# Kernel optimization log

Measured on AMD Instinct MI355X. Metric: run time of the kernel, lower is better.

Reference implementation:

```python
import jax, jax.numpy as jnp
import numpy as np

B, H, S, D = 4, 16, 2048, 128


def setup_inputs() -> dict:
    key = jax.random.key(0)
    kq, kk, kv = jax.random.split(key, 3)
    query = jax.random.normal(kq, (B, H, S, D), dtype=jnp.float32)
    key_t = jax.random.normal(kk, (B, H, S, D), dtype=jnp.float32)
    value = jax.random.normal(kv, (B, H, S, D), dtype=jnp.float32)
    # causal mask, broadcast over batch and heads: True = keep
    mask = jnp.tril(jnp.ones((S, S), dtype=bool))[None, None].repeat(B, 0).repeat(H, 1)
    return {"query": query, "key": key_t, "value": value, "mask": mask}


def reference(query, key, value, mask):
    scale = 1.0 / np.sqrt(D).astype(np.float32)
    # [b,h,sq,sk] scores
    scores = jnp.einsum("bhqd,bhkd->bhqk", query, key) * scale
    scores = jnp.where(mask, scores, -jnp.inf)
    probs = jax.nn.softmax(scores, axis=-1)
    return jnp.einsum("bhqk,bhkd->bhqd", probs, value)
```

## Files before the change

### kernel.cpp

```cpp
#include <hip/hip_runtime.h>


#define SLEN 2048
#define DDIM 128
#define NBH  64
#define QB   256
#define KB   64

typedef __bf16 bf16x8 __attribute__((ext_vector_type(8)));
typedef float  f32x16 __attribute__((ext_vector_type(16)));
typedef float  f32x4  __attribute__((ext_vector_type(4)));
typedef unsigned uint32x4 __attribute__((ext_vector_type(4)));
typedef unsigned short ushort_t;
typedef ushort_t ushort8 __attribute__((ext_vector_type(8)));

__device__ inline ushort_t f2bf(float f) {
  union { float f; unsigned u; } v; v.f = f;
  unsigned u = v.u;
  u += 0x7FFFu + ((u >> 16) & 1u);
  return (ushort_t)(u >> 16);
}

__device__ inline unsigned cvtpk_bf16(float lo, float hi) {
  unsigned r;
  asm("v_cvt_pk_bf16_f32 %0, %1, %2" : "=v"(r) : "v"(lo), "v"(hi));
  return r;
}

__device__ inline float exp2_fast(float x) {
  float r;
  asm("v_exp_f32 %0, %1" : "=v"(r) : "v"(x));
  return r;
}

__global__ __launch_bounds__(256) void prepass_kernel(
    const float* __restrict__ K, const float* __restrict__ V,
    ushort_t* __restrict__ Kb, ushort_t* __restrict__ Vt) {
  __shared__ float t[64][33];
  if (blockIdx.x < 2048) {
    const int n4 = (int)((size_t)NBH * SLEN * DDIM / 4);
    const int stride = 2048 * 256;
    for (int i = blockIdx.x * 256 + threadIdx.x; i < n4; i += stride) {
      float4 x = reinterpret_cast<const float4*>(K)[i];
      unsigned lo = (unsigned)f2bf(x.x) | ((unsigned)f2bf(x.y) << 16);
      unsigned hi = (unsigned)f2bf(x.z) | ((unsigned)f2bf(x.w) << 16);
      reinterpret_cast<uint2*>(Kb)[i] = make_uint2(lo, hi);
    }
  } else {
    const int vb = (int)blockIdx.x - 2048;
    const int bh = vb >> 7;
    const int d0 = ((vb >> 5) & 3) * 32;
    const int s0 = (vb & 31) * 64;
    const int tx = threadIdx.x & 31;
    const int ty = threadIdx.x >> 5;
    const float* src = V + ((size_t)bh * SLEN + s0) * DDIM + d0;
#pragma unroll
    for (int j = 0; j < 8; ++j) {
      int sl = ty + j * 8;
      t[sl][tx] = src[(size_t)sl * DDIM + tx];
    }
    __syncthreads();
    ushort_t* dst = Vt + ((size_t)bh * DDIM + d0) * SLEN + s0;
#pragma unroll
    for (int j = 0; j < 4; ++j) {
      int dl = ty + j * 8;
      unsigned lo = f2bf(t[tx * 2][dl]);
      unsigned hi = f2bf(t[tx * 2 + 1][dl]);
      *reinterpret_cast<unsigned*>(&dst[(size_t)dl * SLEN + tx * 2]) =
          lo | (hi << 16);
    }
  }
}

#define QKT(S, TT) do {                                                      \
    const int _b = (TT) % 3;                                                 \
    _Pragma("unroll")                                                        \
    for (int mt = 0; mt < 2; ++mt) {                                         \
      f32x16 a;                                                              \
      _Pragma("unroll")                                                      \
      for (int r = 0; r < 16; ++r) a[r] = 0.f;                               \
      int row = mt * 32 + l31;                                               \
      int sw = row & 7;                                                      \
      _Pragma("unroll")                                                      \
      for (int ds = 0; ds < 8; ++ds) {                                       \
        int c = ds * 2 + hi;                                                 \
        bf16x8 kf = *reinterpret_cast<const bf16x8*>(                        \
            &K_sh[_b][row * DDIM + ((c ^ sw) << 3)]);                        \
        a = __builtin_amdgcn_mfma_f32_32x32x16_bf16(kf, qf[ds], a, 0, 0, 0); \
      }                                                                      \
      S[mt] = a;                                                             \
    }                                                                        \
  } while (0)

#define FINISH(S, U) do {                                                    \
    const int _u = (U);                                                      \
    const int _vb = _u % 3;                                                  \
    if (_u * 64 + 63 > q0w) {                                                \
      _Pragma("unroll")                                                      \
      for (int mt = 0; mt < 2; ++mt) {                                       \
        int kbase = _u * 64 + mt * 32 + 4 * hi;                              \
        _Pragma("unroll")                                                    \
        for (int r = 0; r < 16; ++r) {                                       \
          int krow = (r & 3) + 8 * (r >> 2);                                 \
          if (kbase + krow > qg) S[mt][r] = -3.0e38f;                        \
        }                                                                    \
      }                                                                      \
    }                                                                        \
    float p0 = S[0][0], p1 = S[0][1], p2 = S[0][2], p3 = S[0][3];            \
    _Pragma("unroll")                                                        \
    for (int r = 4; r < 16; r += 4) {                                        \
      p0 = fmaxf(p0, S[0][r]);     p1 = fmaxf(p1, S[0][r + 1]);              \
      p2 = fmaxf(p2, S[0][r + 2]); p3 = fmaxf(p3, S[0][r + 3]);              \
    }                                                                        \
    _Pragma("unroll")                                                        \
    for (int r = 0; r < 16; r += 4) {                                        \
      p0 = fmaxf(p0, S[1][r]);     p1 = fmaxf(p1, S[1][r + 1]);              \
      p2 = fmaxf(p2, S[1][r + 2]); p3 = fmaxf(p3, S[1][r + 3]);              \
    }                                                                        \
    float tm = fmaxf(fmaxf(p0, p1), fmaxf(p2, p3));                          \
    tm = fmaxf(tm, __shfl_xor(tm, 32));                                      \
    if (!__all(tm - m_run <= THR)) {                                         \
      float mnew  = fmaxf(m_run, tm);                                        \
      float alpha = exp2_fast(m_run - mnew);                                 \
      m_run = mnew; l_run *= alpha;                                          \
      _Pragma("unroll")                                                      \
      for (int dt = 0; dt < 4; ++dt)                                         \
        _Pragma("unroll")                                                    \
        for (int r = 0; r < 16; ++r) Oacc[dt][r] *= alpha;                   \
    }                                                                        \
    float s0 = 0.f, s1 = 0.f, s2 = 0.f, s3 = 0.f;                            \
    _Pragma("unroll")                                                        \
    for (int mt = 0; mt < 2; ++mt)                                           \
      _Pragma("unroll")                                                      \
      for (int r = 0; r < 16; r += 4) {                                      \
        float e0 = exp2_fast(S[mt][r + 0] - m_run);                          \
        float e1 = exp2_fast(S[mt][r + 1] - m_run);                          \
        float e2 = exp2_fast(S[mt][r + 2] - m_run);                          \
        float e3 = exp2_fast(S[mt][r + 3] - m_run);                          \
        S[mt][r + 0] = e0; S[mt][r + 1] = e1;                                \
        S[mt][r + 2] = e2; S[mt][r + 3] = e3;                                \
        s0 += e0; s1 += e1; s2 += e2; s3 += e3;                              \
      }                                                                      \
    float rs = (s0 + s1) + (s2 + s3);                                        \
    rs += __shfl_xor(rs, 32);                                                \
    l_run += rs;                                                             \
    uint32x4 pw[4];                                                          \
    _Pragma("unroll")                                                        \
    for (int ks = 0; ks < 4; ++ks) {                                         \
      const int mt = ks >> 1;                                                \
      const int hb = 8 * (ks & 1);                                           \
      unsigned X  = cvtpk_bf16(S[mt][hb + 0], S[mt][hb + 1]);                \
      unsigned X2 = cvtpk_bf16(S[mt][hb + 2], S[mt][hb + 3]);                \
      unsigned Y  = cvtpk_bf16(S[mt][hb + 4], S[mt][hb + 5]);                \
      unsigned Y2 = cvtpk_bf16(S[mt][hb + 6], S[mt][hb + 7]);                \
      asm("v_permlane32_swap_b32 %0, %1" : "+v"(X),  "+v"(Y));               \
      asm("v_permlane32_swap_b32 %0, %1" : "+v"(X2), "+v"(Y2));              \
      uint32x4 f; f.x = X; f.y = X2; f.z = Y; f.w = Y2;                      \
      pw[ks] = f;                                                            \
    }                                                                        \
    _Pragma("unroll")                                                        \
    for (int dt = 0; dt < 4; ++dt) {                                         \
      int row = dt * 32 + l31;                                               \
      int sw = row & 7;                                                      \
      __builtin_amdgcn_s_setprio(1);                                         \
      _Pragma("unroll")                                                      \
      for (int ks = 0; ks < 4; ++ks) {                                       \
        int c = ks * 2 + hi;                                                 \
        bf16x8 vf = *reinterpret_cast<const bf16x8*>(                        \
            &V_sh[_vb][row * 64 + ((c ^ sw) << 3)]);                         \
        Oacc[dt] = __builtin_amdgcn_mfma_f32_32x32x16_bf16(                  \
            vf, __builtin_bit_cast(bf16x8, pw[ks]), Oacc[dt], 0, 0, 0);      \
      }                                                                      \
      __builtin_amdgcn_s_setprio(0);                                         \
    }                                                                        \
  } while (0)

__global__ __launch_bounds__(512, 1) void fattn6_kernel(
    const float* __restrict__ Q, const ushort_t* __restrict__ Kb,
    const ushort_t* __restrict__ Vt, float* __restrict__ Out) {
  __shared__ ushort_t K_sh[3][KB * DDIM];
  __shared__ ushort_t V_sh[3][DDIM * KB];

  const int tid  = threadIdx.x;
  const int lane = tid & 63;
  const int wv   = tid >> 6;
  const int l31  = lane & 31;
  const int hi   = lane >> 5;
  const int qblk = (blockIdx.y >= 32) ? blockIdx.x : (7 - (int)blockIdx.x);
  const int bh   = blockIdx.y;

  const float qscale = 0.12751744f;
  const float THR = 11.0f;

  const float*    Qp = Q  + (size_t)bh * SLEN * DDIM;
  const ushort_t* Kp = Kb + (size_t)bh * SLEN * DDIM;
  const ushort_t* Vp = Vt + (size_t)bh * DDIM * SLEN;
  float*          Op = Out + (size_t)bh * SLEN * DDIM;

  const int q0w = qblk * QB + wv * 32;
  const int qg  = q0w + l31;

  bf16x8 qf[8];
  {
    const float* qr = Qp + (size_t)qg * DDIM;
#pragma unroll
    for (int ds = 0; ds < 8; ++ds) {
      int d0 = ds * 16 + hi * 8;
      float4 x = *reinterpret_cast<const float4*>(qr + d0);
      float4 y = *reinterpret_cast<const float4*>(qr + d0 + 4);
      ushort8 uu;
      uu[0] = f2bf(x.x * qscale); uu[1] = f2bf(x.y * qscale);
      uu[2] = f2bf(x.z * qscale); uu[3] = f2bf(x.w * qscale);
      uu[4] = f2bf(y.x * qscale); uu[5] = f2bf(y.y * qscale);
      uu[6] = f2bf(y.z * qscale); uu[7] = f2bf(y.w * qscale);
      qf[ds] = __builtin_bit_cast(bf16x8, uu);
    }
  }

  f32x16 Oacc[4];
#pragma unroll
  for (int dt = 0; dt < 4; ++dt)
#pragma unroll
    for (int r = 0; r < 16; ++r) Oacc[dt][r] = 0.f;
  float m_run = -3.0e38f, l_run = 0.f;

  const int last_kb = qblk * 4 + 3;
  const int lkw     = 4 * qblk + (wv >> 1);

  auto stage = [&](int buf, int kb) {
    const ushort_t* ksrc = Kp + (size_t)kb * KB * DDIM;
#pragma unroll
    for (int j = 0; j < 2; ++j) {
      int chunk = wv * 128 + j * 64 + lane;
      int row = chunk >> 4, c = chunk & 15;
      const ushort_t* g = ksrc + row * DDIM + ((c ^ (row & 7)) << 3);
      ushort_t* l = &K_sh[buf][(wv * 128 + j * 64) * 8];
      __builtin_amdgcn_global_load_lds(
          (const __attribute__((address_space(1))) unsigned*)g,
          (__attribute__((address_space(3))) unsigned*)l, 16, 0, 0);
    }
    const ushort_t* vsrc = Vp + (size_t)kb * KB;
#pragma unroll
    for (int j = 0; j < 2; ++j) {
      int chunk = wv * 128 + j * 64 + lane;
      int row = chunk >> 3, c = chunk & 7;
      const ushort_t* g = vsrc + (size_t)row * SLEN + ((c ^ (row & 7)) << 3);
      ushort_t* l = &V_sh[buf][(wv * 128 + j * 64) * 8];
      __builtin_amdgcn_global_load_lds(
          (const __attribute__((address_space(1))) unsigned*)g,
          (__attribute__((address_space(3))) unsigned*)l, 16, 0, 0);
    }
  };

  f32x16 sacA[2], sacB[2];

  stage(0, 0);

  __syncthreads();
  stage(1, 1);
  QKT(sacA, 0);

  __syncthreads();
  if (1 < last_kb) stage(2, 2);
  if (1 <= lkw)           { QKT(sacB, 1); FINISH(sacA, 0); }
  else if (lkw == 0)      { FINISH(sacA, 0); }

  for (int t = 2; t <= last_kb; t += 2) {
    __syncthreads();
    if (t < last_kb) stage((t + 1) % 3, t + 1);
    if (t <= lkw)            { QKT(sacA, t); FINISH(sacB, t - 1); }
    else if (t == lkw + 1)   { FINISH(sacB, t - 1); }

    __syncthreads();
    if (t + 1 < last_kb) stage((t + 2) % 3, t + 2);
    if (t + 1 <= lkw)          { QKT(sacB, t + 1); FINISH(sacA, t); }
    else if (t + 1 == lkw + 1) { FINISH(sacA, t); }
  }

  if (lkw == last_kb) { FINISH(sacB, last_kb); }

  {
    float invl = 1.0f / l_run;
    float* orow = Op + (size_t)qg * DDIM;
#pragma unroll
    for (int dt = 0; dt < 4; ++dt)
#pragma unroll
      for (int rq = 0; rq < 4; ++rq) {
        float4 o;
        o.x = Oacc[dt][rq * 4 + 0] * invl;
        o.y = Oacc[dt][rq * 4 + 1] * invl;
        o.z = Oacc[dt][rq * 4 + 2] * invl;
        o.w = Oacc[dt][rq * 4 + 3] * invl;
        int d = dt * 32 + 8 * rq + 4 * hi;
        *reinterpret_cast<float4*>(orow + d) = o;
      }
  }
}

__global__ __launch_bounds__(256) void fattn_kernel(
    const float* __restrict__ Q, const float* __restrict__ K,
    const float* __restrict__ V, float* __restrict__ Out) {
  __shared__ ushort_t Kf_sh[64 * 128];
  __shared__ ushort_t Vf_sh[128 * 64];
  __shared__ ushort_t P_sh[4][16 * 64];

  const int tid  = threadIdx.x;
  const int lane = tid & 63;
  const int wv   = tid >> 6;
  const int l16  = lane & 15;
  const int lhi  = lane >> 4;
  const int qblk = blockIdx.x;
  const int bh   = blockIdx.y;
  const float scale = 0.08838834764831845f;

  const size_t base = (size_t)bh * SLEN * DDIM;
  const float* Qp = Q + base;
  const float* Kp = K + base;
  const float* Vp = V + base;
  float*       Op = Out + base;

  bf16x8 qf[4];
  {
    const int qrow = qblk * 64 + wv * 16 + l16;
    const float* qr = Qp + (size_t)qrow * DDIM;
#pragma unroll
    for (int dc = 0; dc < 4; ++dc) {
      int d0 = dc * 32 + lhi * 8;
      float4 x = *reinterpret_cast<const float4*>(qr + d0);
      float4 y = *reinterpret_cast<const float4*>(qr + d0 + 4);
      ushort8 uu;
      uu[0] = f2bf(x.x * scale); uu[1] = f2bf(x.y * scale);
      uu[2] = f2bf(x.z * scale); uu[3] = f2bf(x.w * scale);
      uu[4] = f2bf(y.x * scale); uu[5] = f2bf(y.y * scale);
      uu[6] = f2bf(y.z * scale); uu[7] = f2bf(y.w * scale);
      qf[dc] = __builtin_bit_cast(bf16x8, uu);
    }
  }

  f32x4 Oacc[8];
#pragma unroll
  for (int i = 0; i < 8; ++i) Oacc[i] = (f32x4){0.f, 0.f, 0.f, 0.f};
  float m_run[4], l_run[4];
#pragma unroll
  for (int r = 0; r < 4; ++r) { m_run[r] = -3.0e38f; l_run[r] = 0.f; }

  for (int kb = 0; kb <= qblk; ++kb) {
    __syncthreads();
    {
      const float* src = Kp + (size_t)kb * 64 * DDIM;
#pragma unroll
      for (int it = 0; it < 8; ++it) {
        int idx4 = it * 256 + tid;
        int r  = idx4 >> 5;
        int c4 = idx4 & 31;
        float4 x = *reinterpret_cast<const float4*>(src + r * DDIM + c4 * 4);
        unsigned lo = ((unsigned)f2bf(x.y) << 16) | f2bf(x.x);
        unsigned hh = ((unsigned)f2bf(x.w) << 16) | f2bf(x.z);
        int e = (r * 128 + c4 * 4) ^ ((r & 7) << 3);
        *reinterpret_cast<uint2*>(&Kf_sh[e]) = make_uint2(lo, hh);
      }
      const float* vs = Vp + (size_t)kb * 64 * DDIM;
#pragma unroll
      for (int it = 0; it < 8; ++it) {
        int idx4 = it * 256 + tid;
        int r  = idx4 >> 5;
        int c4 = idx4 & 31;
        float4 x = *reinterpret_cast<const float4*>(vs + r * DDIM + c4 * 4);
        int c0 = c4 * 4;
        float vals[4] = {x.x, x.y, x.z, x.w};
#pragma unroll
        for (int j = 0; j < 4; ++j) {
          int d = c0 + j;
          Vf_sh[(d * 64 + r) ^ ((d & 7) << 3)] = f2bf(vals[j]);
        }
      }
    }
    __syncthreads();

    f32x4 sacc[4];
#pragma unroll
    for (int g = 0; g < 4; ++g) {
      f32x4 acc = (f32x4){0.f, 0.f, 0.f, 0.f};
#pragma unroll
      for (int dc = 0; dc < 4; ++dc) {
        int row = g * 16 + l16;
        int e = (row * 128 + dc * 32 + lhi * 8) ^ ((row & 7) << 3);
        bf16x8 kf = *reinterpret_cast<const bf16x8*>(&Kf_sh[e]);
        acc = __builtin_amdgcn_mfma_f32_16x16x32_bf16(qf[dc], kf, acc, 0, 0, 0);
      }
      sacc[g] = acc;
    }

    if (kb == qblk) {
      int q0 = lhi * 4;
#pragma unroll
      for (int g = 0; g < 4; ++g) {
        int kcol = g * 16 + l16;
#pragma unroll
        for (int r = 0; r < 4; ++r) {
          if (kcol > wv * 16 + q0 + r) sacc[g][r] = -3.0e38f;
        }
      }
    }

    float tmax[4];
#pragma unroll
    for (int r = 0; r < 4; ++r)
      tmax[r] = fmaxf(fmaxf(sacc[0][r], sacc[1][r]),
                      fmaxf(sacc[2][r], sacc[3][r]));
#pragma unroll
    for (int x = 1; x < 16; x <<= 1) {
#pragma unroll
      for (int r = 0; r < 4; ++r)
        tmax[r] = fmaxf(tmax[r], __shfl_xor(tmax[r], x));
    }

    float alpha[4], mnew[4];
#pragma unroll
    for (int r = 0; r < 4; ++r) {
      mnew[r]  = fmaxf(m_run[r], tmax[r]);
      alpha[r] = __expf(m_run[r] - mnew[r]);
      m_run[r] = mnew[r];
    }

    float rsum[4] = {0.f, 0.f, 0.f, 0.f};
#pragma unroll
    for (int g = 0; g < 4; ++g) {
#pragma unroll
      for (int r = 0; r < 4; ++r) {
        float p = __expf(sacc[g][r] - mnew[r]);
        rsum[r] += p;
        int prow = lhi * 4 + r;
        P_sh[wv][(prow * 64 + g * 16 + l16) ^ ((prow & 7) << 3)] = f2bf(p);
      }
    }
#pragma unroll
    for (int x = 1; x < 16; x <<= 1) {
#pragma unroll
      for (int r = 0; r < 4; ++r) rsum[r] += __shfl_xor(rsum[r], x);
    }
#pragma unroll
    for (int r = 0; r < 4; ++r) l_run[r] = l_run[r] * alpha[r] + rsum[r];

#pragma unroll
    for (int dg = 0; dg < 8; ++dg)
#pragma unroll
      for (int r = 0; r < 4; ++r) Oacc[dg][r] *= alpha[r];

    bf16x8 pf[2];
#pragma unroll
    for (int kc = 0; kc < 2; ++kc) {
      int e = (l16 * 64 + kc * 32 + lhi * 8) ^ ((l16 & 7) << 3);
      pf[kc] = *reinterpret_cast<const bf16x8*>(&P_sh[wv][e]);
    }
#pragma unroll
    for (int dg = 0; dg < 8; ++dg) {
#pragma unroll
      for (int kc = 0; kc < 2; ++kc) {
        int row = dg * 16 + l16;
        int e = (row * 64 + kc * 32 + lhi * 8) ^ ((row & 7) << 3);
        bf16x8 vf = *reinterpret_cast<const bf16x8*>(&Vf_sh[e]);
        Oacc[dg] = __builtin_amdgcn_mfma_f32_16x16x32_bf16(pf[kc], vf, Oacc[dg], 0, 0, 0);
      }
    }
  }

#pragma unroll
  for (int r = 0; r < 4; ++r) {
    float inv = 1.0f / l_run[r];
    int q = qblk * 64 + wv * 16 + lhi * 4 + r;
    float* orow = Op + (size_t)q * DDIM;
#pragma unroll
    for (int dg = 0; dg < 8; ++dg)
      orow[dg * 16 + l16] = Oacc[dg][r] * inv;
  }
}

extern "C" void kernel_launch(void* const* d_in, const int* in_sizes, int n_in,
                              void* d_out, int out_size, void* d_ws, size_t ws_size,
                              hipStream_t stream) {
  const float* Q = (const float*)d_in[0];
  const float* K = (const float*)d_in[1];
  const float* V = (const float*)d_in[2];
  float* O = (float*)d_out;

  const size_t n_elem = (size_t)NBH * SLEN * DDIM;
  const size_t need   = n_elem * 2 * 2;

  if (ws_size >= need) {
    ushort_t* Kbf = (ushort_t*)d_ws;
    ushort_t* Vt  = Kbf + n_elem;
    prepass_kernel<<<2048 + 8192, 256, 0, stream>>>(K, V, Kbf, Vt);
    fattn6_kernel<<<dim3(SLEN / QB, NBH), dim3(512), 0, stream>>>(Q, Kbf, Vt, O);
  } else {
    fattn_kernel<<<dim3(SLEN / 64, NBH), dim3(256), 0, stream>>>(Q, K, V, O);
  }
}
```

Baseline: 146.0 us.

## Pair mirrored causal query blocks per workgroup to share K/V tiles

Each workgroup now handles two query blocks (xb and 7-xb), so every workgroup does the same amount of causal work and each staged K/V tile serves both blocks. The software pipeline drops from triple-buffered QK/softmax overlap to a simpler double-buffered loop, and launch bounds now allow two workgroups per CU. The grid is halved, which trades the removed load imbalance and redundant K/V loads for higher register pressure (two Q fragment sets and two output accumulators) and the loss of the previous QK^T/softmax overlap.

```diff
diff --git a/kernel.cpp b/kernel.cpp
--- a/kernel.cpp
+++ b/kernel.cpp
@@ -4,7 +4,6 @@
 #define SLEN 2048
 #define DDIM 128
 #define NBH  64
-#define QB   256
 #define KB   64
 
 typedef __bf16 bf16x8 __attribute__((ext_vector_type(8)));
@@ -72,8 +71,7 @@
   }
 }
 
-#define QKT(S, TT) do {                                                      \
-    const int _b = (TT) % 3;                                                 \
+#define QKT_SET(S, QF, BUF) do {                                             \
     _Pragma("unroll")                                                        \
     for (int mt = 0; mt < 2; ++mt) {                                         \
       f32x16 a;                                                              \
@@ -85,24 +83,22 @@
       for (int ds = 0; ds < 8; ++ds) {                                       \
         int c = ds * 2 + hi;                                                 \
         bf16x8 kf = *reinterpret_cast<const bf16x8*>(                        \
-            &K_sh[_b][row * DDIM + ((c ^ sw) << 3)]);                        \
-        a = __builtin_amdgcn_mfma_f32_32x32x16_bf16(kf, qf[ds], a, 0, 0, 0); \
+            &K_sh[BUF][row * DDIM + ((c ^ sw) << 3)]);                       \
+        a = __builtin_amdgcn_mfma_f32_32x32x16_bf16(kf, QF[ds], a, 0, 0, 0); \
       }                                                                      \
       S[mt] = a;                                                             \
     }                                                                        \
   } while (0)
 
-#define FINISH(S, U) do {                                                    \
-    const int _u = (U);                                                      \
-    const int _vb = _u % 3;                                                  \
-    if (_u * 64 + 63 > q0w) {                                                \
+#define FIN_SET(S, U, QG_, Q0W_, MRUN, LRUN, OACC, PW) do {                  \
+    if ((U) * 64 + 63 > (Q0W_)) {                                            \
       _Pragma("unroll")                                                      \
       for (int mt = 0; mt < 2; ++mt) {                                       \
-        int kbase = _u * 64 + mt * 32 + 4 * hi;                              \
+        int kbase = (U) * 64 + mt * 32 + 4 * hi;                             \
         _Pragma("unroll")                                                    \
         for (int r = 0; r < 16; ++r) {                                       \
           int krow = (r & 3) + 8 * (r >> 2);                                 \
-          if (kbase + krow > qg) S[mt][r] = -3.0e38f;                        \
+          if (kbase + krow > (QG_)) S[mt][r] = -3.0e38f;                     \
         }                                                                    \
       }                                                                      \
     }                                                                        \
@@ -119,32 +115,31 @@
     }                                                                        \
     float tm = fmaxf(fmaxf(p0, p1), fmaxf(p2, p3));                          \
     tm = fmaxf(tm, __shfl_xor(tm, 32));                                      \
-    if (!__all(tm - m_run <= THR)) {                                         \
-      float mnew  = fmaxf(m_run, tm);                                        \
-      float alpha = exp2_fast(m_run - mnew);                                 \
-      m_run = mnew; l_run *= alpha;                                          \
+    if (!__all(tm - MRUN <= THR)) {                                          \
+      float mnew  = fmaxf(MRUN, tm);                                         \
+      float alpha = exp2_fast(MRUN - mnew);                                  \
+      MRUN = mnew; LRUN *= alpha;                                            \
       _Pragma("unroll")                                                      \
       for (int dt = 0; dt < 4; ++dt)                                         \
         _Pragma("unroll")                                                    \
-        for (int r = 0; r < 16; ++r) Oacc[dt][r] *= alpha;                   \
+        for (int r = 0; r < 16; ++r) OACC[dt][r] *= alpha;                   \
     }                                                                        \
     float s0 = 0.f, s1 = 0.f, s2 = 0.f, s3 = 0.f;                            \
     _Pragma("unroll")                                                        \
     for (int mt = 0; mt < 2; ++mt)                                           \
       _Pragma("unroll")                                                      \
       for (int r = 0; r < 16; r += 4) {                                      \
-        float e0 = exp2_fast(S[mt][r + 0] - m_run);                          \
-        float e1 = exp2_fast(S[mt][r + 1] - m_run);                          \
-        float e2 = exp2_fast(S[mt][r + 2] - m_run);                          \
-        float e3 = exp2_fast(S[mt][r + 3] - m_run);                          \
+        float e0 = exp2_fast(S[mt][r + 0] - MRUN);                           \
+        float e1 = exp2_fast(S[mt][r + 1] - MRUN);                           \
+        float e2 = exp2_fast(S[mt][r + 2] - MRUN);                           \
+        float e3 = exp2_fast(S[mt][r + 3] - MRUN);                           \
         S[mt][r + 0] = e0; S[mt][r + 1] = e1;                                \
         S[mt][r + 2] = e2; S[mt][r + 3] = e3;                                \
         s0 += e0; s1 += e1; s2 += e2; s3 += e3;                              \
       }                                                                      \
     float rs = (s0 + s1) + (s2 + s3);                                        \
     rs += __shfl_xor(rs, 32);                                                \
-    l_run += rs;                                                             \
-    uint32x4 pw[4];                                                          \
+    LRUN += rs;                                                              \
     _Pragma("unroll")                                                        \
     for (int ks = 0; ks < 4; ++ks) {                                         \
       const int mt = ks >> 1;                                                \
@@ -156,38 +151,26 @@
       asm("v_permlane32_swap_b32 %0, %1" : "+v"(X),  "+v"(Y));               \
       asm("v_permlane32_swap_b32 %0, %1" : "+v"(X2), "+v"(Y2));              \
       uint32x4 f; f.x = X; f.y = X2; f.z = Y; f.w = Y2;                      \
-      pw[ks] = f;                                                            \
-    }                                                                        \
-    _Pragma("unroll")                                                        \
-    for (int dt = 0; dt < 4; ++dt) {                                         \
-      int row = dt * 32 + l31;                                               \
-      int sw = row & 7;                                                      \
-      __builtin_amdgcn_s_setprio(1);                                         \
-      _Pragma("unroll")                                                      \
-      for (int ks = 0; ks < 4; ++ks) {                                       \
-        int c = ks * 2 + hi;                                                 \
-        bf16x8 vf = *reinterpret_cast<const bf16x8*>(                        \
-            &V_sh[_vb][row * 64 + ((c ^ sw) << 3)]);                         \
-        Oacc[dt] = __builtin_amdgcn_mfma_f32_32x32x16_bf16(                  \
-            vf, __builtin_bit_cast(bf16x8, pw[ks]), Oacc[dt], 0, 0, 0);      \
-      }                                                                      \
-      __builtin_amdgcn_s_setprio(0);                                         \
+      PW[ks] = f;                                                            \
     }                                                                        \
   } while (0)
 
-__global__ __launch_bounds__(512, 1) void fattn6_kernel(
+__global__ __launch_bounds__(512, 2) void fattn7_kernel(
     const float* __restrict__ Q, const ushort_t* __restrict__ Kb,
     const ushort_t* __restrict__ Vt, float* __restrict__ Out) {
-  __shared__ ushort_t K_sh[3][KB * DDIM];
-  __shared__ ushort_t V_sh[3][DDIM * KB];
+  __shared__ ushort_t K_sh[2][KB * DDIM];
+  __shared__ ushort_t V_sh[2][DDIM * KB];
 
   const int tid  = threadIdx.x;
   const int lane = tid & 63;
   const int wv   = tid >> 6;
   const int l31  = lane & 31;
   const int hi   = lane >> 5;
-  const int qblk = (blockIdx.y >= 32) ? blockIdx.x : (7 - (int)blockIdx.x);
+  const int xb   = blockIdx.x;
   const int bh   = blockIdx.y;
+
+  const int qblkA = xb;
+  const int qblkB = 7 - xb;
 
   const float qscale = 0.12751744f;
   const float THR = 11.0f;
@@ -197,15 +180,17 @@
   const ushort_t* Vp = Vt + (size_t)bh * DDIM * SLEN;
   float*          Op = Out + (size_t)bh * SLEN * DDIM;
 
-  const int q0w = qblk * QB + wv * 32;
-  const int qg  = q0w + l31;
-
-  bf16x8 qf[8];
-  {
-    const float* qr = Qp + (size_t)qg * DDIM;
-#pragma unroll
-    for (int ds = 0; ds < 8; ++ds) {
-      int d0 = ds * 16 + hi * 8;
+  const int q0wA = qblkA * 256 + wv * 32;
+  const int q0wB = qblkB * 256 + wv * 32;
+  const int qgA  = q0wA + l31;
+  const int qgB  = q0wB + l31;
+
+  bf16x8 qfA[8], qfB[8];
+#pragma unroll
+  for (int ds = 0; ds < 8; ++ds) {
+    int d0 = ds * 16 + hi * 8;
+    {
+      const float* qr = Qp + (size_t)qgA * DDIM;
       float4 x = *reinterpret_cast<const float4*>(qr + d0);
       float4 y = *reinterpret_cast<const float4*>(qr + d0 + 4);
       ushort8 uu;
@@ -213,19 +198,31 @@
       uu[2] = f2bf(x.z * qscale); uu[3] = f2bf(x.w * qscale);
       uu[4] = f2bf(y.x * qscale); uu[5] = f2bf(y.y * qscale);
       uu[6] = f2bf(y.z * qscale); uu[7] = f2bf(y.w * qscale);
-      qf[ds] = __builtin_bit_cast(bf16x8, uu);
-    }
-  }
-
-  f32x16 Oacc[4];
+      qfA[ds] = __builtin_bit_cast(bf16x8, uu);
+    }
+    {
+      const float* qr = Qp + (size_t)qgB * DDIM;
+      float4 x = *reinterpret_cast<const float4*>(qr + d0);
+      float4 y = *reinterpret_cast<const float4*>(qr + d0 + 4);
+      ushort8 uu;
+      uu[0] = f2bf(x.x * qscale); uu[1] = f2bf(x.y * qscale);
+      uu[2] = f2bf(x.z * qscale); uu[3] = f2bf(x.w * qscale);
+      uu[4] = f2bf(y.x * qscale); uu[5] = f2bf(y.y * qscale);
+      uu[6] = f2bf(y.z * qscale); uu[7] = f2bf(y.w * qscale);
+      qfB[ds] = __builtin_bit_cast(bf16x8, uu);
+    }
+  }
+
+  f32x16 OaccA[4], OaccB[4];
 #pragma unroll
   for (int dt = 0; dt < 4; ++dt)
 #pragma unroll
-    for (int r = 0; r < 16; ++r) Oacc[dt][r] = 0.f;
-  float m_run = -3.0e38f, l_run = 0.f;
-
-  const int last_kb = qblk * 4 + 3;
-  const int lkw     = 4 * qblk + (wv >> 1);
+    for (int r = 0; r < 16; ++r) { OaccA[dt][r] = 0.f; OaccB[dt][r] = 0.f; }
+  float mA = -3.0e38f, lA = 0.f, mB = -3.0e38f, lB = 0.f;
+
+  const int last = 4 * qblkB + 3;
+  const int lkwA = 4 * qblkA + (wv >> 1);
+  const int lkwB = 4 * qblkB + (wv >> 1);
 
   auto stage = [&](int buf, int kb) {
     const ushort_t* ksrc = Kp + (size_t)kb * KB * DDIM;
@@ -252,45 +249,88 @@
     }
   };
 
-  f32x16 sacA[2], sacB[2];
-
   stage(0, 0);
 
-  __syncthreads();
-  stage(1, 1);
-  QKT(sacA, 0);
-
-  __syncthreads();
-  if (1 < last_kb) stage(2, 2);
-  if (1 <= lkw)           { QKT(sacB, 1); FINISH(sacA, 0); }
-  else if (lkw == 0)      { FINISH(sacA, 0); }
-
-  for (int t = 2; t <= last_kb; t += 2) {
+  for (int kb = 0; kb <= last; ++kb) {
     __syncthreads();
-    if (t < last_kb) stage((t + 1) % 3, t + 1);
-    if (t <= lkw)            { QKT(sacA, t); FINISH(sacB, t - 1); }
-    else if (t == lkw + 1)   { FINISH(sacB, t - 1); }
-
-    __syncthreads();
-    if (t + 1 < last_kb) stage((t + 2) % 3, t + 2);
-    if (t + 1 <= lkw)          { QKT(sacB, t + 1); FINISH(sacA, t); }
-    else if (t + 1 == lkw + 1) { FINISH(sacA, t); }
-  }
-
-  if (lkw == last_kb) { FINISH(sacB, last_kb); }
+    if (kb < last) stage((kb + 1) & 1, kb + 1);
+    const int buf = kb & 1;
+
+    if (kb <= lkwA) {
+      f32x16 sac[2];
+      uint32x4 pwA[4], pwB[4];
+      QKT_SET(sac, qfB, buf);
+      FIN_SET(sac, kb, qgB, q0wB, mB, lB, OaccB, pwB);
+      QKT_SET(sac, qfA, buf);
+      FIN_SET(sac, kb, qgA, q0wA, mA, lA, OaccA, pwA);
+#pragma unroll
+      for (int dt = 0; dt < 4; ++dt) {
+        int row = dt * 32 + l31;
+        int sw = row & 7;
+        __builtin_amdgcn_s_setprio(1);
+#pragma unroll
+        for (int ks = 0; ks < 4; ++ks) {
+          int c = ks * 2 + hi;
+          bf16x8 vf = *reinterpret_cast<const bf16x8*>(
+              &V_sh[buf][row * 64 + ((c ^ sw) << 3)]);
+          OaccB[dt] = __builtin_amdgcn_mfma_f32_32x32x16_bf16(
+              vf, __builtin_bit_cast(bf16x8, pwB[ks]), OaccB[dt], 0, 0, 0);
+          OaccA[dt] = __builtin_amdgcn_mfma_f32_32x32x16_bf16(
+              vf, __builtin_bit_cast(bf16x8, pwA[ks]), OaccA[dt], 0, 0, 0);
+        }
+        __builtin_amdgcn_s_setprio(0);
+      }
+    } else if (kb <= lkwB) {
+      f32x16 sac[2];
+      uint32x4 pwB[4];
+      QKT_SET(sac, qfB, buf);
+      FIN_SET(sac, kb, qgB, q0wB, mB, lB, OaccB, pwB);
+#pragma unroll
+      for (int dt = 0; dt < 4; ++dt) {
+        int row = dt * 32 + l31;
+        int sw = row & 7;
+        __builtin_amdgcn_s_setprio(1);
+#pragma unroll
+        for (int ks = 0; ks < 4; ++ks) {
+          int c = ks * 2 + hi;
+          bf16x8 vf = *reinterpret_cast<const bf16x8*>(
+              &V_sh[buf][row * 64 + ((c ^ sw) << 3)]);
+          OaccB[dt] = __builtin_amdgcn_mfma_f32_32x32x16_bf16(
+              vf, __builtin_bit_cast(bf16x8, pwB[ks]), OaccB[dt], 0, 0, 0);
+        }
+        __builtin_amdgcn_s_setprio(0);
+      }
+    }
+  }
 
   {
-    float invl = 1.0f / l_run;
-    float* orow = Op + (size_t)qg * DDIM;
+    float invA = 1.0f / lA;
+    float* orow = Op + (size_t)qgA * DDIM;
 #pragma unroll
     for (int dt = 0; dt < 4; ++dt)
 #pragma unroll
       for (int rq = 0; rq < 4; ++rq) {
         float4 o;
-        o.x = Oacc[dt][rq * 4 + 0] * invl;
-        o.y = Oacc[dt][rq * 4 + 1] * invl;
-        o.z = Oacc[dt][rq * 4 + 2] * invl;
-        o.w = Oacc[dt][rq * 4 + 3] * invl;
+        o.x = OaccA[dt][rq * 4 + 0] * invA;
+        o.y = OaccA[dt][rq * 4 + 1] * invA;
+        o.z = OaccA[dt][rq * 4 + 2] * invA;
+        o.w = OaccA[dt][rq * 4 + 3] * invA;
+        int d = dt * 32 + 8 * rq + 4 * hi;
+        *reinterpret_cast<float4*>(orow + d) = o;
+      }
+  }
+  {
+    float invB = 1.0f / lB;
+    float* orow = Op + (size_t)qgB * DDIM;
+#pragma unroll
+    for (int dt = 0; dt < 4; ++dt)
+#pragma unroll
+      for (int rq = 0; rq < 4; ++rq) {
+        float4 o;
+        o.x = OaccB[dt][rq * 4 + 0] * invB;
+        o.y = OaccB[dt][rq * 4 + 1] * invB;
+        o.z = OaccB[dt][rq * 4 + 2] * invB;
+        o.w = OaccB[dt][rq * 4 + 3] * invB;
         int d = dt * 32 + 8 * rq + 4 * hi;
         *reinterpret_cast<float4*>(orow + d) = o;
       }
@@ -491,7 +531,7 @@
     ushort_t* Kbf = (ushort_t*)d_ws;
     ushort_t* Vt  = Kbf + n_elem;
     prepass_kernel<<<2048 + 8192, 256, 0, stream>>>(K, V, Kbf, Vt);
-    fattn6_kernel<<<dim3(SLEN / QB, NBH), dim3(512), 0, stream>>>(Q, Kbf, Vt, O);
+    fattn7_kernel<<<dim3(4, NBH), dim3(512), 0, stream>>>(Q, Kbf, Vt, O);
   } else {
     fattn_kernel<<<dim3(SLEN / 64, NBH), dim3(256), 0, stream>>>(Q, K, V, O);
   }
```

New measurement: 217.2 us. 48.7% more time.
